# Kernel tuning notes

Hardware: AMD Instinct MI355X
Metric: run time of the kernel (lower is better)

## Reference

```python
import jax, jax.numpy as jnp
import numpy as np

T, KBLK, EMB, B = 2048, 64, 512, 4


def _make_coords(t, k):
    # head1: for each j, cols = block_start(j) + arange(j % k + 1)  (block-causal local)
    j = np.arange(t)
    cnt1 = (j % k) + 1
    rows1 = np.repeat(j, cnt1)
    off1 = np.arange(cnt1.sum()) - np.repeat(np.cumsum(cnt1) - cnt1, cnt1)
    cols1 = (rows1 // k) * k + off1
    # head2: for each block start c, rows = arange(c, t), col = c  (strided block-start)
    starts = np.arange(t // k) * k
    cnt2 = t - starts
    base = np.repeat(starts, cnt2)
    off2 = np.arange(cnt2.sum()) - np.repeat(np.cumsum(cnt2) - cnt2, cnt2)
    rows2, cols2 = base + off2, base
    c1 = np.stack([rows1, cols1], 1).astype(np.int32)
    c2 = np.stack([rows2, cols2], 1).astype(np.int32)
    return c1, c2


def setup_inputs() -> dict:
    key = jax.random.key(0)
    ks = jax.random.split(key, 6)
    s = 1.0 / float(np.sqrt(EMB))
    c1, c2 = _make_coords(T, KBLK)
    return {
        "x": jax.random.normal(ks[0], (B, T, EMB), jnp.float32),
        "Wk": jax.random.normal(ks[1], (EMB, EMB), jnp.float32) * s,
        "bk": jnp.zeros((EMB,), jnp.float32),
        "Wq": jax.random.normal(ks[2], (EMB, EMB), jnp.float32) * s,
        "bq": jnp.zeros((EMB,), jnp.float32),
        "Wv": jax.random.normal(ks[3], (EMB, EMB), jnp.float32) * s,
        "bv": jnp.zeros((EMB,), jnp.float32),
        "Wu": jax.random.normal(ks[4], (EMB, 2 * EMB), jnp.float32) * s,
        "bu": jnp.zeros((EMB,), jnp.float32),
        "coords1": jnp.asarray(c1),
        "coords2": jnp.asarray(c2),
    }


def _sparse_head(Kt, Qt, Vt, coords):
    rows, cols = coords[:, 0], coords[:, 1]
    # dot[b,p] = (K @ Q^T)[b, rows[p], cols[p]] = K[b,rows[p],:] . Q[b,cols[p],:]
    dot = jnp.einsum('bpe,bpe->bp', Kt[:, rows], Qt[:, cols])
    # sparse.batchmm: out[b,r] = sum_{p: rows[p]=r} dot[b,p] * V[b, cols[p]]
    out = jnp.zeros_like(Vt).at[:, rows].add(dot[..., None] * Vt[:, cols])
    return out


def reference(x, Wk, bk, Wq, bq, Wv, bv, Wu, bu, coords1, coords2):
    Kt = x @ Wk.T + bk
    Qt = x @ Wq.T + bq
    Vt = x @ Wv.T + bv
    h1 = _sparse_head(Kt, Qt, Vt, coords1)
    h2 = _sparse_head(Kt, Qt, Vt, coords2)
    comb = jnp.concatenate([h1, h2], axis=-1)  # [B, T, 2*EMB]
    return comb @ Wu.T + bu
```

## Files before the change

kernel.cpp:

```cpp
#include <hip/hip_runtime.h>


typedef unsigned short u16;
typedef __attribute__((ext_vector_type(8))) short short8;
typedef __attribute__((ext_vector_type(4))) float f32x4;

constexpr int TDIM  = 2048;
constexpr int EMB_D = 512;
constexpr int BB    = 4;
constexpr int NBLK  = 32;
constexpr int LDK   = 2048;

__device__ __forceinline__ u16 f2b(float f) {
    unsigned u = __float_as_uint(f);
    unsigned r = (u + 0x7FFFu + ((u >> 16) & 1u)) >> 16;
    return (u16)r;
}

__global__ __launch_bounds__(256) void prep_k(
    const float* __restrict__ x, const float* __restrict__ Wk, const float* __restrict__ Wq,
    const float* __restrict__ Wv, const float* __restrict__ Wu,
    const float* __restrict__ bk, const float* __restrict__ bq, const float* __restrict__ bv,
    u16* __restrict__ xb, u16* __restrict__ wcat, float* __restrict__ biascat)
{
    const int bid = blockIdx.x, tid = threadIdx.x;
    if (bid < 32) {
        const int bm = (bid >> 2) * 128;
        const int bn = (bid & 3) * 128;
        const int wid  = tid >> 6;
        const int lane = tid & 63;
        const int l15  = lane & 15;
        const int quad = lane >> 4;
        const int wm = (wid & 1) * 64;
        const int wn = (wid >> 1) * 64;

        f32x4 acc[4][4] = {};

        const float* Arow[4];
        #pragma unroll
        for (int i = 0; i < 4; ++i) {
            const int m = bm + wm + 16 * i + l15;
            Arow[i] = Wu + (size_t)(m & 511) * 1024 + (m >> 9) * 512 + quad * 8;
        }
        const float* Bcol[4];
        #pragma unroll
        for (int g = 0; g < 4; ++g)
            Bcol[g] = Wv + (bn + wn + 16 * g + l15) + (size_t)(quad * 8) * 512;

        for (int j0 = 0; j0 < 512; j0 += 32) {
            short8 a[4], b[4];
            #pragma unroll
            for (int i = 0; i < 4; ++i) {
                float4 v0 = *(const float4*)(Arow[i] + j0);
                float4 v1 = *(const float4*)(Arow[i] + j0 + 4);
                a[i] = (short8){(short)f2b(v0.x), (short)f2b(v0.y), (short)f2b(v0.z), (short)f2b(v0.w),
                                (short)f2b(v1.x), (short)f2b(v1.y), (short)f2b(v1.z), (short)f2b(v1.w)};
            }
            #pragma unroll
            for (int g = 0; g < 4; ++g) {
                const float* p = Bcol[g] + (size_t)j0 * 512;
                float v0 = p[0];          float v1 = p[512];
                float v2 = p[1024];       float v3 = p[1536];
                float v4 = p[2048];       float v5 = p[2560];
                float v6 = p[3072];       float v7 = p[3584];
                b[g] = (short8){(short)f2b(v0), (short)f2b(v1), (short)f2b(v2), (short)f2b(v3),
                                (short)f2b(v4), (short)f2b(v5), (short)f2b(v6), (short)f2b(v7)};
            }
            #pragma unroll
            for (int i = 0; i < 4; ++i)
                #pragma unroll
                for (int g = 0; g < 4; ++g)
                    acc[i][g] = __builtin_amdgcn_mfma_f32_16x16x32_bf16(a[i], b[g], acc[i][g], 0, 0, 0);
        }

        #pragma unroll
        for (int i = 0; i < 4; ++i)
            #pragma unroll
            for (int g = 0; g < 4; ++g) {
                const int col = bn + wn + 16 * g + l15;
                #pragma unroll
                for (int r = 0; r < 4; ++r) {
                    const int row = bm + wm + 16 * i + quad * 4 + r;
                    wcat[(size_t)(1024 + row) * 512 + col] = f2b(acc[i][g][r]);
                }
            }
    } else if (bid < 4640) {
        const float* src; u16* dst; int base;
        if (bid < 4128)      { src = x;  dst = xb;            base = (bid - 32) * 1024; }
        else if (bid < 4384) { src = Wk; dst = wcat;          base = (bid - 4128) * 1024; }
        else                 { src = Wq; dst = wcat + 262144; base = (bid - 4384) * 1024; }
        const int idx = base + tid * 4;
        float4 v = *(const float4*)(src + idx);
        ushort4 o = { f2b(v.x), f2b(v.y), f2b(v.z), f2b(v.w) };
        *(ushort4*)(dst + idx) = o;
    } else if (bid < 4656) {
        const int o = (bid - 4640) * 64 + (tid >> 2);
        const int p = tid & 3;
        const int n = o & 511, half = o >> 9;
        const float* wr = Wu + (size_t)n * 1024 + half * 512 + p * 128;
        const float* br = bv + p * 128;
        float s = 0.f;
        #pragma unroll
        for (int j = 0; j < 128; j += 4) {
            float4 a = *(const float4*)(wr + j);
            float4 b = *(const float4*)(br + j);
            s += a.x*b.x + a.y*b.y + a.z*b.z + a.w*b.w;
        }
        s += __shfl_xor(s, 1);
        s += __shfl_xor(s, 2);
        if (p == 0) biascat[1024 + o] = s;
    } else {
        const int idx = tid * 4;
        float4 v = (idx < 512) ? *(const float4*)(bk + idx)
                               : *(const float4*)(bq + idx - 512);
        *(float4*)(biascat + idx) = v;
    }
}

template<int MH, int KK>
__device__ __forceinline__ void mm16(const short8 (&a)[4], const short8 (&b)[2][4],
                                     f32x4 (&acc)[8][4])
{
    #pragma unroll
    for (int f = 0; f < 4; ++f)
        #pragma unroll
        for (int g = 0; g < 4; ++g)
            acc[MH * 4 + f][g] = __builtin_amdgcn_mfma_f32_16x16x32_bf16(
                a[f], b[KK][g], acc[MH * 4 + f][g], 0, 0, 0);
}

template<int SLOT, int MH>
__device__ __forceinline__ void lda4(short8 (&a)[4], const u16* sm, int arow, int koff)
{
    #pragma unroll
    for (int f = 0; f < 4; ++f)
        a[f] = *(const short8*)(sm + SLOT * 32768 + (arow + MH * 64 + f * 16) * 64 + koff);
}

template<int SLOT>
__device__ __forceinline__ void ldb4(short8 (&bk)[4], const u16* sm, int brow, int koff)
{
    #pragma unroll
    for (int g = 0; g < 4; ++g)
        bk[g] = *(const short8*)(sm + SLOT * 32768 + 16384 + (brow + g * 16) * 64 + koff);
}

#define STA(S, CI, T) __builtin_amdgcn_global_load_lds( \
    (const __attribute__((address_space(1))) void*)(Ag + (size_t)(CI) * 32768 + (T) * 64), \
    (__attribute__((address_space(3))) void*)(sm + (S) * 32768 + (CI) * 4096 + wid * 512), 16, 0, 0)
#define STB(S, CI, T) __builtin_amdgcn_global_load_lds( \
    (const __attribute__((address_space(1))) void*)(Bg + (size_t)(CI) * 32768 + (T) * 64), \
    (__attribute__((address_space(3))) void*)(sm + (S) * 32768 + 16384 + (CI) * 4096 + wid * 512), 16, 0, 0)
#define KBAR()  __builtin_amdgcn_s_barrier()
#define KPRIO(P) __builtin_amdgcn_s_setprio(P)
#define LGKM0() do { asm volatile("s_waitcnt lgkmcnt(0)" ::: "memory"); \
                     __builtin_amdgcn_sched_barrier(0); } while (0)
#define VMC4()  asm volatile("s_waitcnt vmcnt(4)" ::: "memory")
#define VMC0()  asm volatile("s_waitcnt vmcnt(0)" ::: "memory")

__global__ __launch_bounds__(512, 2) void kqv_gemm_k(
    const u16* __restrict__ A, const u16* __restrict__ W,
    const float* __restrict__ bias, u16* __restrict__ C)
{
    __shared__ u16 sm[65536];

    const int bid = blockIdx.x;
    const int wg  = (bid & 7) * 32 + (bid >> 3);
    const int bm  = (wg & 31) * 256;
    const int bn  = (wg >> 5) * 256;
    const int tid  = threadIdx.x;
    const int wid  = tid >> 6;
    const int lane = tid & 63;
    const int l15  = lane & 15;
    const int quad = lane >> 4;
    const int wm = wid >> 2;
    const int wn = wid & 3;

    const int stgrow = wid * 8 + (lane >> 3);
    const int stgk   = ((lane & 7) ^ ((lane >> 3) & 7)) << 3;
    const u16* Ag = A + (size_t)(bm + stgrow) * 512 + stgk;
    const u16* Bg = W + (size_t)(bn + stgrow) * 512 + stgk;

    const int r7     = l15 & 7;
    const int arow   = wm * 128 + l15;
    const int brow   = wn * 64 + l15;
    const int off_k0 = ((quad ^ r7) << 3);
    const int off_k1 = (((4 | quad) ^ r7) << 3);

    f32x4 acc[8][4] = {};
    short8 a[4], b[2][4];

    STA(0,0,0); STA(0,2,0); STB(0,0,0); STB(0,1,0);
    STB(0,2,0); STB(0,3,0); STA(0,1,0); STA(0,3,0);
    STA(1,0,1); STA(1,2,1); STB(1,0,1); STB(1,1,1);
    VMC4(); KBAR();

    for (int it = 0; it < 3; ++it) {
        const int t = 2 * it;
        ldb4<0>(b[0], sm, brow, off_k0); lda4<0,0>(a, sm, arow, off_k0);
        STB(1,2,t+1); STB(1,3,t+1);
        KBAR(); LGKM0(); KPRIO(1); mm16<0,0>(a, b, acc); KPRIO(0); KBAR();
        ldb4<0>(b[1], sm, brow, off_k1); lda4<0,0>(a, sm, arow, off_k1);
        STA(1,1,t+1); STA(1,3,t+1);
        KBAR(); LGKM0(); KPRIO(1); mm16<0,1>(a, b, acc); KPRIO(0); KBAR();
        lda4<0,1>(a, sm, arow, off_k0);
        STA(0,0,t+2); STA(0,2,t+2);
        KBAR(); LGKM0(); KPRIO(1); mm16<1,0>(a, b, acc); KPRIO(0); KBAR();
        lda4<0,1>(a, sm, arow, off_k1);
        STB(0,0,t+2); STB(0,1,t+2);
        KBAR(); LGKM0(); KPRIO(1); mm16<1,1>(a, b, acc); KPRIO(0); VMC4(); KBAR();
        ldb4<1>(b[0], sm, brow, off_k0); lda4<1,0>(a, sm, arow, off_k0);
        STB(0,2,t+2); STB(0,3,t+2);
        KBAR(); LGKM0(); KPRIO(1); mm16<0,0>(a, b, acc); KPRIO(0); KBAR();
        ldb4<1>(b[1], sm, brow, off_k1); lda4<1,0>(a, sm, arow, off_k1);
        STA(0,1,t+2); STA(0,3,t+2);
        KBAR(); LGKM0(); KPRIO(1); mm16<0,1>(a, b, acc); KPRIO(0); KBAR();
        lda4<1,1>(a, sm, arow, off_k0);
        STA(1,0,t+3); STA(1,2,t+3);
        KBAR(); LGKM0(); KPRIO(1); mm16<1,0>(a, b, acc); KPRIO(0); KBAR();
        lda4<1,1>(a, sm, arow, off_k1);
        STB(1,0,t+3); STB(1,1,t+3);
        KBAR(); LGKM0(); KPRIO(1); mm16<1,1>(a, b, acc); KPRIO(0); VMC4(); KBAR();
    }

    ldb4<0>(b[0], sm, brow, off_k0); lda4<0,0>(a, sm, arow, off_k0);
    STB(1,2,7); STB(1,3,7);
    KBAR(); LGKM0(); KPRIO(1); mm16<0,0>(a, b, acc); KPRIO(0); KBAR();
    ldb4<0>(b[1], sm, brow, off_k1); lda4<0,0>(a, sm, arow, off_k1);
    STA(1,1,7); STA(1,3,7);
    KBAR(); LGKM0(); KPRIO(1); mm16<0,1>(a, b, acc); KPRIO(0); KBAR();
    lda4<0,1>(a, sm, arow, off_k0);
    KBAR(); LGKM0(); KPRIO(1); mm16<1,0>(a, b, acc); KPRIO(0); KBAR();
    lda4<0,1>(a, sm, arow, off_k1);
    KBAR(); LGKM0(); KPRIO(1); mm16<1,1>(a, b, acc); KPRIO(0); VMC0(); KBAR();
    ldb4<1>(b[0], sm, brow, off_k0); lda4<1,0>(a, sm, arow, off_k0);
    KBAR(); LGKM0(); KPRIO(1); mm16<0,0>(a, b, acc); KPRIO(0); KBAR();
    ldb4<1>(b[1], sm, brow, off_k1); lda4<1,0>(a, sm, arow, off_k1);
    KBAR(); LGKM0(); KPRIO(1); mm16<0,1>(a, b, acc); KPRIO(0); KBAR();
    lda4<1,1>(a, sm, arow, off_k0);
    KBAR(); LGKM0(); KPRIO(1); mm16<1,0>(a, b, acc); KPRIO(0); KBAR();
    lda4<1,1>(a, sm, arow, off_k1);
    KBAR(); LGKM0(); KPRIO(1); mm16<1,1>(a, b, acc); KPRIO(0);

    __syncthreads();
    #pragma unroll
    for (int mf = 0; mf < 8; ++mf) {
        #pragma unroll
        for (int g = 0; g < 4; ++g) {
            const int col = wn * 64 + g * 16 + l15;
            const float bvv = bias[bn + col];
            #pragma unroll
            for (int r = 0; r < 4; ++r) {
                const int row = wm * 128 + mf * 16 + quad * 4 + r;
                sm[row * 256 + col] = f2b(acc[mf][g][r] + bvv);
            }
        }
    }
    __syncthreads();
    {
        const int rr = tid >> 5;
        const int ck = tid & 31;
        #pragma unroll
        for (int p = 0; p < 16; ++p) {
            const int row = p * 16 + rr;
            short8 v = *(const short8*)(sm + row * 256 + ck * 8);
            *(short8*)(C + (size_t)(bm + row) * LDK + bn + ck * 8) = v;
        }
    }
}

#undef STA
#undef STB
#undef KBAR
#undef KPRIO
#undef LGKM0
#undef VMC4
#undef VMC0

__global__ __launch_bounds__(256) void heads_k(
    const u16* __restrict__ KQV, const float* __restrict__ bu, float* __restrict__ out)
{
    __shared__ u16 smA[64 * 104];
    __shared__ u16 smVT[128 * 104];
    __shared__ u16 pK[2][64 * 32];
    __shared__ u16 pQ[2][64 * 32];
    __shared__ u16 pQs[2][32 * 32];

    const int blk = blockIdx.x, b = blockIdx.y;
    const int e0 = blockIdx.z * 128;
    const int tid = threadIdx.x;
    const int wid = tid >> 6, lane = tid & 63;
    const int l15 = lane & 15, quad = lane >> 4;
    const size_t row0 = (size_t)b * TDIM + (size_t)blk * 64;
    const size_t brow = (size_t)b * TDIM;
    const int srow_base = 16 * wid + quad * 4;

    #pragma unroll
    for (int it = 0; it < 4; ++it) {
        const int id = tid + 256 * it;
        const int c  = id & 63;
        const int eo = (id >> 6) * 8;
        short8 v = *(const short8*)(KQV + (row0 + c) * (size_t)LDK + 1024 + e0 + eo);
        #pragma unroll
        for (int i = 0; i < 8; ++i) smVT[(eo + i) * 104 + c] = (u16)v[i];
    }
    #pragma unroll
    for (int it = 0; it < 2; ++it) {
        const int id = tid + 256 * it;
        const int m  = id & 31;
        const int eo = (id >> 5) * 8;
        short8 v = *(const short8*)(KQV + (brow + 64 * m) * (size_t)LDK + 1536 + e0 + eo);
        #pragma unroll
        for (int i = 0; i < 8; ++i) smVT[(eo + i) * 104 + 64 + m] = (u16)v[i];
    }

    f32x4 s1[4] = {}; f32x4 s2[2] = {};
    const int srow  = tid >> 2;
    const int skoff = (tid & 3) * 8;
    const int qsrow = srow & 31;
    const int qsp   = tid >> 7;
    const u16* Kg  = KQV + (row0 + srow) * (size_t)LDK + skoff;
    const u16* Qg  = KQV + (row0 + srow) * (size_t)LDK + 512 + skoff;
    const u16* Qsg = KQV + (brow + (size_t)64 * qsrow) * (size_t)LDK + 512 + qsp * 32 + skoff;
    char* dK  = (char*)pK  + wid * 1024;
    char* dQ  = (char*)pQ  + wid * 1024;
    char* dQs = (char*)pQs + wid * 1024;

    for (int k0 = 0; k0 < 512; k0 += 64) {
        __syncthreads();
        __builtin_amdgcn_global_load_lds(
            (const __attribute__((address_space(1))) void*)(Kg + k0),
            (__attribute__((address_space(3))) void*)dK, 16, 0, 0);
        __builtin_amdgcn_global_load_lds(
            (const __attribute__((address_space(1))) void*)(Kg + k0 + 32),
            (__attribute__((address_space(3))) void*)(dK + 4096), 16, 0, 0);
        __builtin_amdgcn_global_load_lds(
            (const __attribute__((address_space(1))) void*)(Qg + k0),
            (__attribute__((address_space(3))) void*)dQ, 16, 0, 0);
        __builtin_amdgcn_global_load_lds(
            (const __attribute__((address_space(1))) void*)(Qg + k0 + 32),
            (__attribute__((address_space(3))) void*)(dQ + 4096), 16, 0, 0);
        __builtin_amdgcn_global_load_lds(
            (const __attribute__((address_space(1))) void*)(Qsg + k0),
            (__attribute__((address_space(3))) void*)dQs, 16, 0, 0);
        __syncthreads();

        short8 a0 = *(const short8*)(pK[0] + (16 * wid + l15) * 32 + quad * 8);
        short8 a1 = *(const short8*)(pK[1] + (16 * wid + l15) * 32 + quad * 8);
        #pragma unroll
        for (int j = 0; j < 4; ++j) {
            short8 b0 = *(const short8*)(pQ[0] + (16 * j + l15) * 32 + quad * 8);
            short8 b1 = *(const short8*)(pQ[1] + (16 * j + l15) * 32 + quad * 8);
            s1[j] = __builtin_amdgcn_mfma_f32_16x16x32_bf16(a0, b0, s1[j], 0, 0, 0);
            s1[j] = __builtin_amdgcn_mfma_f32_16x16x32_bf16(a1, b1, s1[j], 0, 0, 0);
        }
        #pragma unroll
        for (int j = 0; j < 2; ++j) {
            short8 b0 = *(const short8*)(pQs[0] + (16 * j + l15) * 32 + quad * 8);
            short8 b1 = *(const short8*)(pQs[1] + (16 * j + l15) * 32 + quad * 8);
            s2[j] = __builtin_amdgcn_mfma_f32_16x16x32_bf16(a0, b0, s2[j], 0, 0, 0);
            s2[j] = __builtin_amdgcn_mfma_f32_16x16x32_bf16(a1, b1, s2[j], 0, 0, 0);
        }
    }

    #pragma unroll
    for (int j = 0; j < 4; ++j)
        #pragma unroll
        for (int r = 0; r < 4; ++r) {
            const int rr = srow_base + r;
            const int cc = 16 * j + l15;
            smA[rr * 104 + cc] = f2b((cc <= rr) ? s1[j][r] : 0.0f);
        }
    #pragma unroll
    for (int j = 0; j < 2; ++j)
        #pragma unroll
        for (int r = 0; r < 4; ++r) {
            const int m  = 16 * j + l15;
            const int rr = srow_base + r;
            smA[rr * 104 + 64 + m] = f2b((m <= blk) ? s2[j][r] : 0.0f);
        }
    __syncthreads();

    f32x4 o[8] = {};
    const u16* arow = smA + (16 * wid + l15) * 104;
    #pragma unroll
    for (int ks = 0; ks < 3; ++ks) {
        short8 as = *(const short8*)(arow + 32 * ks + quad * 8);
        #pragma unroll
        for (int nt = 0; nt < 8; ++nt) {
            short8 bs = *(const short8*)(smVT + (16 * nt + l15) * 104 + 32 * ks + quad * 8);
            o[nt] = __builtin_amdgcn_mfma_f32_16x16x32_bf16(as, bs, o[nt], 0, 0, 0);
        }
    }
    #pragma unroll
    for (int nt = 0; nt < 8; ++nt) {
        const int col = e0 + 16 * nt + l15;
        const float bvv = bu[col];
        #pragma unroll
        for (int r = 0; r < 4; ++r)
            out[(row0 + srow_base + r) * (size_t)EMB_D + col] = o[nt][r] + bvv;
    }
}

extern "C" void kernel_launch(void* const* d_in, const int* in_sizes, int n_in,
                              void* d_out, int out_size, void* d_ws, size_t ws_size,
                              hipStream_t stream)
{
    const float* x  = (const float*)d_in[0];
    const float* Wk = (const float*)d_in[1];
    const float* bk = (const float*)d_in[2];
    const float* Wq = (const float*)d_in[3];
    const float* bq = (const float*)d_in[4];
    const float* Wv = (const float*)d_in[5];
    const float* bv = (const float*)d_in[6];
    const float* Wu = (const float*)d_in[7];
    const float* bu = (const float*)d_in[8];
    float* out = (float*)d_out;

    char* w = (char*)d_ws;
    u16*   KQV     = (u16*)  (w + ((size_t)0  << 20));
    u16*   xb      = (u16*)  (w + ((size_t)32 << 20));
    u16*   wcat    = (u16*)  (w + ((size_t)40 << 20));
    float* biascat = (float*)(w + ((size_t)44 << 20));

    hipLaunchKernelGGL(prep_k, dim3(4657), dim3(256), 0, stream,
                       x, Wk, Wq, Wv, Wu, bk, bq, bv, xb, wcat, biascat);
    hipLaunchKernelGGL(kqv_gemm_k, dim3(256), dim3(512), 0, stream, xb, wcat, biascat, KQV);
    hipLaunchKernelGGL(heads_k, dim3(NBLK, BB, 4), dim3(256), 0, stream, KQV, bu, out);
}
```

Before: 141.6 us.

## Widen heads kernel to 512 threads covering 256 output columns per block

```diff
diff --git a/kernel.cpp b/kernel.cpp
--- a/kernel.cpp
+++ b/kernel.cpp
@@ -277,27 +277,28 @@
 #undef VMC4
 #undef VMC0
 
-__global__ __launch_bounds__(256) void heads_k(
+__global__ __launch_bounds__(512) void heads_k(
     const u16* __restrict__ KQV, const float* __restrict__ bu, float* __restrict__ out)
 {
     __shared__ u16 smA[64 * 104];
-    __shared__ u16 smVT[128 * 104];
+    __shared__ u16 smVT[256 * 104];
     __shared__ u16 pK[2][64 * 32];
     __shared__ u16 pQ[2][64 * 32];
     __shared__ u16 pQs[2][32 * 32];
 
     const int blk = blockIdx.x, b = blockIdx.y;
-    const int e0 = blockIdx.z * 128;
+    const int e0 = blockIdx.z * 256;
     const int tid = threadIdx.x;
     const int wid = tid >> 6, lane = tid & 63;
     const int l15 = lane & 15, quad = lane >> 4;
+    const int rw = wid & 3, ch = wid >> 2;
     const size_t row0 = (size_t)b * TDIM + (size_t)blk * 64;
     const size_t brow = (size_t)b * TDIM;
-    const int srow_base = 16 * wid + quad * 4;
+    const int srow_base = 16 * rw + quad * 4;
 
     #pragma unroll
     for (int it = 0; it < 4; ++it) {
-        const int id = tid + 256 * it;
+        const int id = tid + 512 * it;
         const int c  = id & 63;
         const int eo = (id >> 6) * 8;
         short8 v = *(const short8*)(KQV + (row0 + c) * (size_t)LDK + 1024 + e0 + eo);
@@ -306,7 +307,7 @@
     }
     #pragma unroll
     for (int it = 0; it < 2; ++it) {
-        const int id = tid + 256 * it;
+        const int id = tid + 512 * it;
         const int m  = id & 31;
         const int eo = (id >> 5) * 8;
         short8 v = *(const short8*)(KQV + (brow + 64 * m) * (size_t)LDK + 1536 + e0 + eo);
@@ -314,14 +315,15 @@
         for (int i = 0; i < 8; ++i) smVT[(eo + i) * 104 + 64 + m] = (u16)v[i];
     }
 
-    f32x4 s1[4] = {}; f32x4 s2[2] = {};
-    const int srow  = tid >> 2;
-    const int skoff = (tid & 3) * 8;
-    const int qsrow = srow & 31;
-    const int qsp   = tid >> 7;
-    const u16* Kg  = KQV + (row0 + srow) * (size_t)LDK + skoff;
-    const u16* Qg  = KQV + (row0 + srow) * (size_t)LDK + 512 + skoff;
-    const u16* Qsg = KQV + (brow + (size_t)64 * qsrow) * (size_t)LDK + 512 + qsp * 32 + skoff;
+    f32x4 s1[2] = {}; f32x4 s2 = {};
+    const int strow  = (tid >> 2) & 63;
+    const int sthalf = tid >> 8;
+    const int stk    = (tid & 3) * 8;
+    const u16* Kg = KQV + (row0 + strow) * (size_t)LDK + sthalf * 32 + stk;
+    const u16* Qg = Kg + 512;
+    const int qrow  = (tid >> 2) & 31;
+    const int qhalf = (tid >> 7) & 1;
+    const u16* Qsg = KQV + (brow + (size_t)64 * qrow) * (size_t)LDK + 512 + qhalf * 32 + stk;
     char* dK  = (char*)pK  + wid * 1024;
     char* dQ  = (char*)pQ  + wid * 1024;
     char* dQs = (char*)pQs + wid * 1024;
@@ -332,69 +334,62 @@
             (const __attribute__((address_space(1))) void*)(Kg + k0),
             (__attribute__((address_space(3))) void*)dK, 16, 0, 0);
         __builtin_amdgcn_global_load_lds(
-            (const __attribute__((address_space(1))) void*)(Kg + k0 + 32),
-            (__attribute__((address_space(3))) void*)(dK + 4096), 16, 0, 0);
-        __builtin_amdgcn_global_load_lds(
             (const __attribute__((address_space(1))) void*)(Qg + k0),
             (__attribute__((address_space(3))) void*)dQ, 16, 0, 0);
-        __builtin_amdgcn_global_load_lds(
-            (const __attribute__((address_space(1))) void*)(Qg + k0 + 32),
-            (__attribute__((address_space(3))) void*)(dQ + 4096), 16, 0, 0);
-        __builtin_amdgcn_global_load_lds(
-            (const __attribute__((address_space(1))) void*)(Qsg + k0),
-            (__attribute__((address_space(3))) void*)dQs, 16, 0, 0);
+        if (wid < 4)
+            __builtin_amdgcn_global_load_lds(
+                (const __attribute__((address_space(1))) void*)(Qsg + k0),
+                (__attribute__((address_space(3))) void*)dQs, 16, 0, 0);
         __syncthreads();
 
-        short8 a0 = *(const short8*)(pK[0] + (16 * wid + l15) * 32 + quad * 8);
-        short8 a1 = *(const short8*)(pK[1] + (16 * wid + l15) * 32 + quad * 8);
-        #pragma unroll
-        for (int j = 0; j < 4; ++j) {
+        short8 a0 = *(const short8*)(pK[0] + (16 * rw + l15) * 32 + quad * 8);
+        short8 a1 = *(const short8*)(pK[1] + (16 * rw + l15) * 32 + quad * 8);
+        #pragma unroll
+        for (int jj = 0; jj < 2; ++jj) {
+            const int j = 2 * ch + jj;
             short8 b0 = *(const short8*)(pQ[0] + (16 * j + l15) * 32 + quad * 8);
             short8 b1 = *(const short8*)(pQ[1] + (16 * j + l15) * 32 + quad * 8);
-            s1[j] = __builtin_amdgcn_mfma_f32_16x16x32_bf16(a0, b0, s1[j], 0, 0, 0);
-            s1[j] = __builtin_amdgcn_mfma_f32_16x16x32_bf16(a1, b1, s1[j], 0, 0, 0);
-        }
-        #pragma unroll
-        for (int j = 0; j < 2; ++j) {
-            short8 b0 = *(const short8*)(pQs[0] + (16 * j + l15) * 32 + quad * 8);
-            short8 b1 = *(const short8*)(pQs[1] + (16 * j + l15) * 32 + quad * 8);
-            s2[j] = __builtin_amdgcn_mfma_f32_16x16x32_bf16(a0, b0, s2[j], 0, 0, 0);
-            s2[j] = __builtin_amdgcn_mfma_f32_16x16x32_bf16(a1, b1, s2[j], 0, 0, 0);
-        }
-    }
-
-    #pragma unroll
-    for (int j = 0; j < 4; ++j)
+            s1[jj] = __builtin_amdgcn_mfma_f32_16x16x32_bf16(a0, b0, s1[jj], 0, 0, 0);
+            s1[jj] = __builtin_amdgcn_mfma_f32_16x16x32_bf16(a1, b1, s1[jj], 0, 0, 0);
+        }
+        {
+            short8 b0 = *(const short8*)(pQs[0] + (16 * ch + l15) * 32 + quad * 8);
+            short8 b1 = *(const short8*)(pQs[1] + (16 * ch + l15) * 32 + quad * 8);
+            s2 = __builtin_amdgcn_mfma_f32_16x16x32_bf16(a0, b0, s2, 0, 0, 0);
+            s2 = __builtin_amdgcn_mfma_f32_16x16x32_bf16(a1, b1, s2, 0, 0, 0);
+        }
+    }
+
+    #pragma unroll
+    for (int jj = 0; jj < 2; ++jj)
         #pragma unroll
         for (int r = 0; r < 4; ++r) {
             const int rr = srow_base + r;
-            const int cc = 16 * j + l15;
-            smA[rr * 104 + cc] = f2b((cc <= rr) ? s1[j][r] : 0.0f);
-        }
-    #pragma unroll
-    for (int j = 0; j < 2; ++j)
-        #pragma unroll
-        for (int r = 0; r < 4; ++r) {
-            const int m  = 16 * j + l15;
-            const int rr = srow_base + r;
-            smA[rr * 104 + 64 + m] = f2b((m <= blk) ? s2[j][r] : 0.0f);
-        }
+            const int cc = 32 * ch + 16 * jj + l15;
+            smA[rr * 104 + cc] = f2b((cc <= rr) ? s1[jj][r] : 0.0f);
+        }
+    #pragma unroll
+    for (int r = 0; r < 4; ++r) {
+        const int m  = 16 * ch + l15;
+        const int rr = srow_base + r;
+        smA[rr * 104 + 64 + m] = f2b((m <= blk) ? s2[r] : 0.0f);
+    }
     __syncthreads();
 
     f32x4 o[8] = {};
-    const u16* arow = smA + (16 * wid + l15) * 104;
+    const u16* arow = smA + (16 * rw + l15) * 104;
     #pragma unroll
     for (int ks = 0; ks < 3; ++ks) {
         short8 as = *(const short8*)(arow + 32 * ks + quad * 8);
         #pragma unroll
         for (int nt = 0; nt < 8; ++nt) {
-            short8 bs = *(const short8*)(smVT + (16 * nt + l15) * 104 + 32 * ks + quad * 8);
+            short8 bs = *(const short8*)(smVT + (16 * (8 * ch + nt) + l15) * 104 + 32 * ks + quad * 8);
             o[nt] = __builtin_amdgcn_mfma_f32_16x16x32_bf16(as, bs, o[nt], 0, 0, 0);
         }
     }
     #pragma unroll
     for (int nt = 0; nt < 8; ++nt) {
-        const int col = e0 + 16 * nt + l15;
+        const int col = e0 + 16 * (8 * ch + nt) + l15;
         const float bvv = bu[col];
         #pragma unroll
         for (int r = 0; r < 4; ++r)
@@ -426,5 +421,5 @@
     hipLaunchKernelGGL(prep_k, dim3(4657), dim3(256), 0, stream,
                        x, Wk, Wq, Wv, Wu, bk, bq, bv, xb, wcat, biascat);
     hipLaunchKernelGGL(kqv_gemm_k, dim3(256), dim3(512), 0, stream, xb, wcat, biascat, KQV);
-    hipLaunchKernelGGL(heads_k, dim3(NBLK, BB, 4), dim3(256), 0, stream, KQV, bu, out);
-}
+    hipLaunchKernelGGL(heads_k, dim3(NBLK, BB, 2), dim3(512), 0, stream, KQV, bu, out);
+}
```

Measured after the change: 141.5 us. About the same (-0.1%).
